# Optimization experiments

Hardware: AMD Instinct MI355X
Metric: run time of the kernel (lower is better)

## Reference

```python
import jax, jax.numpy as jnp
import numpy as np
import math

NUM_HEADS = 8
LN_EPS = 1e-5


def layer_norm(x, g, b):
    mu = x.mean(-1, keepdims=True)
    var = ((x - mu) ** 2).mean(-1, keepdims=True)
    return (x - mu) * jax.lax.rsqrt(var + LN_EPS) * g + b


def typed_linear(x, W, types):
    # x: [E, in], W: [R, in, out], types: [E] int -> [E, out]
    out = jnp.zeros((x.shape[0], W.shape[-1]), x.dtype)
    for r in range(W.shape[0]):  # small fixed relation count
        out = out + jnp.where((types == r)[:, None], x @ W[r], 0.0)
    return out


def setup_inputs() -> dict:
    key = jax.random.key(0)
    ks = jax.random.split(key, 20)
    N, M, E = 50000, 10000, 100000
    in_dim, e_dim, out_dim, td = 128, 32, 128, 32
    R, T = 8, 4
    inp = {
        'src_h': jax.random.normal(ks[0], (N, in_dim), jnp.float32),
        'src_tw': jax.random.normal(ks[1], (N, td), jnp.float32),
        'src_tb': jax.random.normal(ks[2], (N, td), jnp.float32),
        'edge_h': jax.random.normal(ks[3], (E, e_dim), jnp.float32),
        'date': jax.random.uniform(ks[4], (E,), jnp.float32),
        'src_idx': jax.random.randint(ks[5], (E,), 0, N, jnp.int32),
        'dst_idx': jax.random.randint(ks[6], (E,), 0, M, jnp.int32),
        'etype': jax.random.randint(ks[7], (E,), 0, R, jnp.int32),
        'ntype': jax.random.randint(ks[8], (M,), 0, T, jnp.int32),
    }
    def w(k, shape):
        return jax.random.normal(k, shape, jnp.float32) / math.sqrt(shape[-2])
    inp['Wq'] = w(ks[9], (R, in_dim, out_dim))
    inp['Wk'] = w(ks[10], (R, in_dim + e_dim, out_dim))
    inp['Wv'] = w(ks[11], (R, in_dim + e_dim, out_dim))
    inp['Wa'] = w(ks[12], (T, out_dim, out_dim))
    inp['h_bias'] = jnp.zeros((T, out_dim), jnp.float32)
    inp['skip'] = jnp.ones((T,), jnp.float32)
    inp['src_ln_g'] = jnp.ones((in_dim + e_dim,), jnp.float32)
    inp['src_ln_b'] = jnp.zeros((in_dim + e_dim,), jnp.float32)
    inp['dst_ln_g'] = jnp.ones((in_dim,), jnp.float32)
    inp['dst_ln_b'] = jnp.zeros((in_dim,), jnp.float32)
    return inp


def reference(src_h, src_tw, src_tb, edge_h, date, src_idx, dst_idx, etype, ntype,
              Wq, Wk, Wv, Wa, h_bias, skip, src_ln_g, src_ln_b, dst_ln_g, dst_ln_b):
    M = ntype.shape[0]
    out_dim = Wq.shape[-1]
    H = NUM_HEADS
    hs = out_dim // H
    td = src_tw.shape[-1]
    t = date[:, None]  # [E,1]

    # gather src / dst node data per edge (dst nodes are first M src rows)
    h_s, tw_s, tb_s = src_h[src_idx], src_tw[src_idx], src_tb[src_idx]
    h_d, tw_d, tb_d = src_h[dst_idx], src_tw[dst_idx], src_tb[dst_idx]

    # time2vec modulation of the first td channels
    dia_s = jnp.concatenate([jnp.sin(tw_s * t + tb_s) * h_s[:, :td], h_s[:, td:]], -1)
    dia_d = jnp.concatenate([jnp.sin(tw_d * t + tb_d) * h_d[:, :td], h_d[:, td:]], -1)
    dia_s = jnp.concatenate([dia_s, edge_h], -1)  # [E, in_dim+e_dim]

    # pre_norm
    dia_s = layer_norm(dia_s, src_ln_g, src_ln_b)
    dia_d = layer_norm(dia_d, dst_ln_g, dst_ln_b)

    q = typed_linear(dia_d, Wq, etype).reshape(-1, H, hs)
    k = typed_linear(dia_s, Wk, etype).reshape(-1, H, hs)
    v = typed_linear(dia_s, Wv, etype).reshape(-1, H, hs)

    a = (q * k).sum(-1) / math.sqrt(out_dim)  # [E, H]

    # edge_softmax: segment softmax over destination nodes
    amax = jax.lax.stop_gradient(jax.ops.segment_max(a, dst_idx, num_segments=M))
    ex = jnp.exp(a - amax[dst_idx])
    denom = jax.ops.segment_sum(ex, dst_idx, num_segments=M)
    alpha = ex / denom[dst_idx]  # [E, H]

    # weighted scatter-sum aggregation
    m = (v * alpha[..., None]).reshape(-1, out_dim)  # [E, out_dim]
    h = jax.ops.segment_sum(m, dst_idx, num_segments=M)  # [M, out_dim]

    h = h + h_bias[ntype]
    gate = jax.nn.sigmoid(skip[ntype])[:, None]
    h = typed_linear(h, Wa, ntype)  # dropout is identity at eval
    dst_h = src_h[:M]
    return h * gate + dst_h * (1.0 - gate)
```

## Files before the change

kernel.cpp:

```cpp
#include <hip/hip_runtime.h>


typedef __attribute__((ext_vector_type(8))) short short8;
typedef __attribute__((ext_vector_type(4))) float f32x4;

__device__ __forceinline__ unsigned short f2bf(float f){
  union { float f; unsigned u; } x; x.f = f;
  unsigned r = x.u + 0x7FFFu + ((x.u >> 16) & 1u);
  return (unsigned short)(r >> 16);
}
__device__ __forceinline__ float bf2f(unsigned short b){
  union { unsigned u; float f; } x; x.u = ((unsigned)b) << 16;
  return x.f;
}
__device__ __forceinline__ float wred(float v){
  #pragma unroll
  for(int i=1;i<64;i<<=1) v += __shfl_xor(v, i);
  return v;
}


__global__ void k_zero(int* __restrict__ p, int n){
  int i = blockIdx.x*256 + threadIdx.x;
  if(i < n) p[i] = 0;
}

__global__ __launch_bounds__(256) void k_hist(
    const int* __restrict__ etype, const int* __restrict__ dst_idx,
    const int* __restrict__ ntype,
    int* cnt_e, int* cnt_d, int* cnt_n, int E, int M){
  __shared__ int le[8], ln[4];
  int tid = threadIdx.x;
  if(tid < 8) le[tid] = 0;
  if(tid < 4) ln[tid] = 0;
  __syncthreads();
  int g = blockIdx.x*256 + tid;
  if(g < E){ atomicAdd(&le[etype[g]], 1); atomicAdd(&cnt_d[dst_idx[g]], 1); }
  if(g < M){ atomicAdd(&ln[ntype[g]], 1); }
  __syncthreads();
  if(tid < 8 && le[tid]) atomicAdd(&cnt_e[tid], le[tid]);
  if(tid < 4 && ln[tid]) atomicAdd(&cnt_n[tid], ln[tid]);
}

__global__ __launch_bounds__(1024) void k_scan(const int* __restrict__ cnt_e, int* off_e,
                                               const int* __restrict__ cnt_n, int* off_n,
                                               const int* __restrict__ cnt_d, int* off_d, int M){
  __shared__ int part[1024];
  int tid = threadIdx.x;
  if(tid == 0){
    int s = 0;
    for(int i=0;i<8;i++){ off_e[i]=s; s+=cnt_e[i]; } off_e[8]=s;
    s = 0;
    for(int i=0;i<4;i++){ off_n[i]=s; s+=cnt_n[i]; } off_n[4]=s;
  }
  int per = (M + 1023) >> 10;
  int s = 0;
  for(int j=0;j<per;j++){ int idx = tid*per + j; if(idx < M) s += cnt_d[idx]; }
  part[tid] = s; __syncthreads();
  for(int o=1;o<1024;o<<=1){
    int v = (tid >= o) ? part[tid-o] : 0;
    __syncthreads();
    part[tid] += v;
    __syncthreads();
  }
  int run = (tid == 0) ? 0 : part[tid-1];
  for(int j=0;j<per;j++){
    int idx = tid*per + j;
    if(idx < M){ off_d[idx] = run; run += cnt_d[idx]; }
  }
  if(tid == 1023) off_d[M] = run;
}

__global__ __launch_bounds__(256) void k_scatter(
    const int* __restrict__ etype, const int* __restrict__ dst_idx,
    const int* __restrict__ ntype,
    const int* __restrict__ off_e, int* cur_e,
    const int* __restrict__ off_d, int* cur_d,
    const int* __restrict__ off_n, int* cur_n,
    int* eperm, int* dstlist, int* nperm, int* npos, int E, int M){
  __shared__ int lcnt[8], lbase[8], lnc[4], lnb[4];
  int tid = threadIdx.x;
  if(tid < 8) lcnt[tid] = 0;
  if(tid < 4) lnc[tid] = 0;
  __syncthreads();
  int g = blockIdx.x*256 + tid;
  int r = 0, lrank = 0, t = 0, nrank = 0;
  bool inE = (g < E), inM = (g < M);
  if(inE){ r = etype[g]; lrank = atomicAdd(&lcnt[r], 1); }
  if(inM){ t = ntype[g]; nrank = atomicAdd(&lnc[t], 1); }
  __syncthreads();
  if(tid < 8 && lcnt[tid]) lbase[tid] = atomicAdd(&cur_e[tid], lcnt[tid]);
  if(tid < 4 && lnc[tid])  lnb[tid]   = atomicAdd(&cur_n[tid], lnc[tid]);
  __syncthreads();
  if(inE){
    int p = off_e[r] + lbase[r] + lrank;
    eperm[p] = g;
    int d = dst_idx[g];
    int q = off_d[d] + atomicAdd(&cur_d[d], 1);
    dstlist[q] = p;
  }
  if(inM){
    int np = off_n[t] + lnb[t] + nrank;
    npos[g] = np;
    nperm[np] = g;
  }
}

__global__ void k_convw(const float* __restrict__ Wq, const float* __restrict__ Wk,
                        const float* __restrict__ Wv, const float* __restrict__ Wa,
                        unsigned short* Wq_t, unsigned short* Wk_t,
                        unsigned short* Wv_t, unsigned short* Wa_t){
  int tid = blockIdx.x*256 + threadIdx.x;
  if(tid < 131072){
    int r = tid >> 14, rem = tid & 16383, k = rem >> 7, n = rem & 127;
    int nb=n>>4, m=n&15, c=k>>5, quad=(k>>3)&3, j=k&7;
    Wq_t[r*16384 + ((nb*4 + c)*4 + quad)*128 + m*8 + j] = f2bf(Wq[tid]);
  } else if(tid < 294912){
    int u = tid - 131072;
    int r = u / 20480, rem = u - r*20480, k = rem >> 7, n = rem & 127;
    int nb=n>>4, m=n&15, c=k>>5, quad=(k>>3)&3, j=k&7;
    Wk_t[r*20480 + ((nb*5 + c)*4 + quad)*128 + m*8 + j] = f2bf(Wk[u]);
  } else if(tid < 458752){
    int u = tid - 294912;
    int r = u / 20480, rem = u - r*20480, k = rem >> 7, n = rem & 127;
    int nb=n>>4, m=n&15, c=k>>5, quad=(k>>3)&3, j=k&7;
    Wv_t[r*20480 + ((nb*5 + c)*4 + quad)*128 + m*8 + j] = f2bf(Wv[u]);
  } else if(tid < 524288){
    int u = tid - 458752;
    int r = u >> 14, rem = u & 16383, k = rem >> 7, n = rem & 127;
    int nb=n>>4, m=n&15, c=k>>5, quad=(k>>3)&3, j=k&7;
    Wa_t[r*16384 + ((nb*4 + c)*4 + quad)*128 + m*8 + j] = f2bf(Wa[u]);
  }
}

__global__ __launch_bounds__(256) void k_prep(
  const float* __restrict__ src_h, const float* __restrict__ src_tw, const float* __restrict__ src_tb,
  const float* __restrict__ edge_h, const float* __restrict__ date,
  const int* __restrict__ src_idx, const int* __restrict__ dst_idx, const int* __restrict__ eperm,
  const float* __restrict__ g_s, const float* __restrict__ b_s,
  const float* __restrict__ g_d, const float* __restrict__ b_d,
  unsigned short* __restrict__ dia_s, unsigned short* __restrict__ dia_d, int E)
{
  int p = blockIdx.x*4 + (threadIdx.x >> 6);
  if(p >= E) return;
  int lane = threadIdx.x & 63;
  int e = eperm[p];
  float t = date[e];
  int s = src_idx[e], d = dst_idx[e];
  {
    float h0 = src_h[(size_t)s*128 + lane];
    float h1 = src_h[(size_t)s*128 + 64 + lane];
    float x0 = h0, x2 = 0.f;
    if(lane < 32){
      x0 = __sinf(src_tw[s*32 + lane]*t + src_tb[s*32 + lane]) * h0;
      x2 = edge_h[(size_t)e*32 + lane];
    }
    float x1 = h1;
    float mu = wred(x0 + x1 + x2) * (1.f/160.f);
    float d0 = x0-mu, d1 = x1-mu, d2 = (lane<32) ? (x2-mu) : 0.f;
    float var = wred(d0*d0 + d1*d1 + d2*d2) * (1.f/160.f);
    float sc = rsqrtf(var + 1e-5f);
    size_t bo = (size_t)p*160;
    dia_s[bo + lane]      = f2bf(d0*sc*g_s[lane]      + b_s[lane]);
    dia_s[bo + 64 + lane] = f2bf(d1*sc*g_s[64+lane]   + b_s[64+lane]);
    if(lane < 32)
      dia_s[bo + 128 + lane] = f2bf(d2*sc*g_s[128+lane] + b_s[128+lane]);
  }
  {
    float h0 = src_h[(size_t)d*128 + lane];
    float h1 = src_h[(size_t)d*128 + 64 + lane];
    float x0 = (lane < 32) ? __sinf(src_tw[d*32+lane]*t + src_tb[d*32+lane]) * h0 : h0;
    float x1 = h1;
    float mu = wred(x0 + x1) * (1.f/128.f);
    float d0 = x0-mu, d1 = x1-mu;
    float var = wred(d0*d0 + d1*d1) * (1.f/128.f);
    float sc = rsqrtf(var + 1e-5f);
    size_t bo = (size_t)p*128;
    dia_d[bo + lane]      = f2bf(d0*sc*g_d[lane]    + b_d[lane]);
    dia_d[bo + 64 + lane] = f2bf(d1*sc*g_d[64+lane] + b_d[64+lane]);
  }
}

template<int NC>
__device__ __forceinline__ void gemm64r(
  const unsigned short* __restrict__ A, int lda,
  const unsigned short* __restrict__ Wf,
  f32x4* acc, int tid)
{
  int lane = tid & 63, w = tid >> 6, m = lane & 15, quad = lane >> 4;
  const unsigned short* p0 = Wf + (size_t)(2*w)*NC*512 + lane*8;
  short8 b0[NC], b1[NC];
  #pragma unroll
  for(int c=0;c<NC;c++){
    b0[c] = *(const short8*)(p0 + c*512);
    b1[c] = *(const short8*)(p0 + NC*512 + c*512);
  }
  #pragma unroll
  for(int i=0;i<8;i++) acc[i] = (f32x4){0.f,0.f,0.f,0.f};
  #pragma unroll
  for(int c=0;c<NC;c++){
    #pragma unroll
    for(int rt=0; rt<4; rt++){
      short8 af = *(const short8*)(A + (rt*16 + m)*lda + c*32 + quad*8);
      acc[rt*2+0] = __builtin_amdgcn_mfma_f32_16x16x32_bf16(af, b0[c], acc[rt*2+0], 0,0,0);
      acc[rt*2+1] = __builtin_amdgcn_mfma_f32_16x16x32_bf16(af, b1[c], acc[rt*2+1], 0,0,0);
    }
  }
}

__global__ __launch_bounds__(256) void k_qkv(
  const unsigned short* __restrict__ dia_d, const unsigned short* __restrict__ dia_s,
  const unsigned short* __restrict__ Wq_t, const unsigned short* __restrict__ Wk_t,
  const unsigned short* __restrict__ Wv_t,
  const int* __restrict__ cnt_e, const int* __restrict__ off_e,
  float* __restrict__ abuf, unsigned short* __restrict__ vbuf)
{
  __shared__ unsigned short Ad[64*136];
  __shared__ unsigned short As[64*168];
  int bid = blockIdx.x;
  int r = -1, tl0 = 0, accT = 0;
  #pragma unroll
  for(int i=0;i<8;i++){
    int n = cnt_e[i], tt = (n + 63) >> 6;
    if(r < 0 && bid < accT + tt){ r = i; tl0 = bid - accT; }
    accT += tt;
  }
  if(r < 0) return;
  int row0 = off_e[r] + tl0*64;
  int nv = min(64, cnt_e[r] - tl0*64);
  int tid = threadIdx.x;
  {
    int4 z = make_int4(0,0,0,0);
    #pragma unroll
    for(int it=0; it<4; it++){
      int idx = it*256 + tid, row = idx >> 4, c = idx & 15;
      int4 v = z;
      if(row < nv) v = *(const int4*)(dia_d + (size_t)(row0+row)*128 + c*8);
      *(int4*)(Ad + row*136 + c*8) = v;
    }
    #pragma unroll
    for(int it=0; it<5; it++){
      int idx = it*256 + tid, row = idx/20, c = idx%20;
      int4 v = z;
      if(row < nv) v = *(const int4*)(dia_s + (size_t)(row0+row)*160 + c*8);
      *(int4*)(As + row*168 + c*8) = v;
    }
  }
  __syncthreads();
  int lane = tid & 63, w = tid >> 6, m = lane & 15, quad = lane >> 4;
  f32x4 q[8], kk[8], vv[8];
  gemm64r<4>(Ad, 136, Wq_t + r*16384, q,  tid);
  gemm64r<5>(As, 168, Wk_t + r*20480, kk, tid);
  const float inv = 0.08838834764831845f;
  #pragma unroll
  for(int rt=0; rt<4; rt++)
  #pragma unroll
  for(int ct=0; ct<2; ct++){
    #pragma unroll
    for(int reg=0; reg<4; reg++){
      float s = q[rt*2+ct][reg] * kk[rt*2+ct][reg];
      s += __shfl_xor(s,1); s += __shfl_xor(s,2); s += __shfl_xor(s,4); s += __shfl_xor(s,8);
      int row = rt*16 + quad*4 + reg;
      if(m == 0 && row < nv) abuf[(size_t)(row0+row)*8 + w*2 + ct] = s * inv;
    }
  }
  gemm64r<5>(As, 168, Wv_t + r*20480, vv, tid);
  #pragma unroll
  for(int rt=0; rt<4; rt++)
  #pragma unroll
  for(int ct=0; ct<2; ct++)
  #pragma unroll
  for(int reg=0; reg<4; reg++){
    int row = rt*16 + quad*4 + reg;
    if(row < nv)
      vbuf[(size_t)(row0+row)*128 + w*32 + ct*16 + m] = f2bf(vv[rt*2+ct][reg]);
  }
}

__global__ __launch_bounds__(128) void k_aggr(
  const float* __restrict__ abuf, const unsigned short* __restrict__ vbuf,
  const int* __restrict__ dstlist, const int* __restrict__ off_d,
  const int* __restrict__ npos, const int* __restrict__ ntype,
  const float* __restrict__ h_bias, unsigned short* __restrict__ hpre)
{
  int d = blockIdx.x, tid = threadIdx.x;
  int o0 = off_d[d], cnt = off_d[d+1] - o0;
  __shared__ float den[8];
  if(tid < 8) den[tid] = 0.f;
  __syncthreads();
  for(int idx = tid; idx < cnt*8; idx += 128){
    int i = idx >> 3, h = idx & 7;
    float ex = __expf(abuf[(size_t)dstlist[o0+i]*8 + h]);
    atomicAdd(&den[h], ex);
  }
  __syncthreads();
  int h = tid >> 4;
  float dh = den[h];
  float rd = (dh > 0.f) ? (1.f/dh) : 0.f;
  float acc = 0.f;
  for(int i=0; i<cnt; i++){
    int p = dstlist[o0+i];
    float al = __expf(abuf[(size_t)p*8 + h]) * rd;
    acc += al * bf2f(vbuf[(size_t)p*128 + tid]);
  }
  int t = ntype[d];
  acc += h_bias[t*128 + tid];
  hpre[(size_t)npos[d]*128 + tid] = f2bf(acc);
}

__global__ __launch_bounds__(256) void k_final(
  const unsigned short* __restrict__ hpre, const unsigned short* __restrict__ Wa_t,
  const int* __restrict__ cnt_n, const int* __restrict__ off_n, const int* __restrict__ nperm,
  const float* __restrict__ skip, const float* __restrict__ src_h, float* __restrict__ out)
{
  __shared__ unsigned short Ah[64*136];
  int bid = blockIdx.x;
  int r = -1, tl0 = 0, accT = 0;
  #pragma unroll
  for(int i=0;i<4;i++){
    int n = cnt_n[i], tt = (n + 63) >> 6;
    if(r < 0 && bid < accT + tt){ r = i; tl0 = bid - accT; }
    accT += tt;
  }
  if(r < 0) return;
  int row0 = off_n[r] + tl0*64;
  int nv = min(64, cnt_n[r] - tl0*64);
  float gate = 1.f / (1.f + __expf(-skip[r]));
  int tid = threadIdx.x;
  int4 z = make_int4(0,0,0,0);
  #pragma unroll
  for(int it=0; it<4; it++){
    int idx = it*256 + tid, row = idx >> 4, c = idx & 15;
    int4 v = z;
    if(row < nv) v = *(const int4*)(hpre + (size_t)(row0+row)*128 + c*8);
    *(int4*)(Ah + row*136 + c*8) = v;
  }
  __syncthreads();
  f32x4 acc[8];
  gemm64r<4>(Ah, 136, Wa_t + r*16384, acc, tid);
  int lane = tid & 63, w = tid >> 6, m = lane & 15, quad = lane >> 4;
  #pragma unroll
  for(int rt=0; rt<4; rt++)
  #pragma unroll
  for(int ct=0; ct<2; ct++)
  #pragma unroll
  for(int reg=0; reg<4; reg++){
    int row = rt*16 + quad*4 + reg;
    if(row < nv){
      int dd = nperm[row0+row];
      int col = w*32 + ct*16 + m;
      out[(size_t)dd*128 + col] = acc[rt*2+ct][reg]*gate + src_h[(size_t)dd*128 + col]*(1.f - gate);
    }
  }
}

extern "C" void kernel_launch(void* const* d_in, const int* in_sizes, int n_in,
                              void* d_out, int out_size, void* d_ws, size_t ws_size,
                              hipStream_t stream)
{
  const float* src_h  = (const float*)d_in[0];
  const float* src_tw = (const float*)d_in[1];
  const float* src_tb = (const float*)d_in[2];
  const float* edge_h = (const float*)d_in[3];
  const float* date   = (const float*)d_in[4];
  const int*   src_idx= (const int*)d_in[5];
  const int*   dst_idx= (const int*)d_in[6];
  const int*   etype  = (const int*)d_in[7];
  const int*   ntype  = (const int*)d_in[8];
  const float* Wq     = (const float*)d_in[9];
  const float* Wk     = (const float*)d_in[10];
  const float* Wv     = (const float*)d_in[11];
  const float* Wa     = (const float*)d_in[12];
  const float* h_bias = (const float*)d_in[13];
  const float* skip   = (const float*)d_in[14];
  const float* g_s    = (const float*)d_in[15];
  const float* b_s    = (const float*)d_in[16];
  const float* g_d    = (const float*)d_in[17];
  const float* b_d    = (const float*)d_in[18];
  float* out = (float*)d_out;

  const int E = in_sizes[4];
  const int M = in_sizes[8];

  char* base = (char*)d_ws;
  size_t off = 0;
  auto alloc = [&](size_t bytes)->char*{
    off = (off + 255) & ~(size_t)255;
    char* p = base + off; off += bytes; return p;
  };
  int* cnt_e = (int*)alloc((size_t)(24 + 2*M)*4);
  int* cur_e = cnt_e + 8;
  int* cnt_n = cur_e + 8;
  int* cur_n = cnt_n + 4;
  int* cnt_d = cur_n + 4;
  int* cur_d = cnt_d + M;
  const int nzero = 24 + 2*M;
  int* off_e = (int*)alloc(9*4);
  int* off_n = (int*)alloc(5*4);
  int* off_d = (int*)alloc((size_t)(M+1)*4);
  int* eperm   = (int*)alloc((size_t)E*4);
  int* dstlist = (int*)alloc((size_t)E*4);
  int* nperm   = (int*)alloc((size_t)M*4);
  int* npos    = (int*)alloc((size_t)M*4);
  unsigned short* Wq_t = (unsigned short*)alloc((size_t)8*128*128*2);
  unsigned short* Wk_t = (unsigned short*)alloc((size_t)8*160*128*2);
  unsigned short* Wv_t = (unsigned short*)alloc((size_t)8*160*128*2);
  unsigned short* Wa_t = (unsigned short*)alloc((size_t)4*128*128*2);
  unsigned short* dia_d = (unsigned short*)alloc((size_t)E*128*2);
  unsigned short* dia_s = (unsigned short*)alloc((size_t)E*160*2);
  unsigned short* vbuf  = (unsigned short*)alloc((size_t)E*128*2);
  unsigned short* hpre  = (unsigned short*)alloc((size_t)M*128*2);
  float* abuf = (float*)alloc((size_t)E*8*4);

  k_zero<<<dim3((nzero+255)/256), dim3(256), 0, stream>>>(cnt_e, nzero);
  k_hist<<<dim3((E+255)/256), dim3(256), 0, stream>>>(etype, dst_idx, ntype, cnt_e, cnt_d, cnt_n, E, M);
  k_scan<<<dim3(1), dim3(1024), 0, stream>>>(cnt_e, off_e, cnt_n, off_n, cnt_d, off_d, M);
  k_scatter<<<dim3((E+255)/256), dim3(256), 0, stream>>>(etype, dst_idx, ntype,
      off_e, cur_e, off_d, cur_d, off_n, cur_n, eperm, dstlist, nperm, npos, E, M);
  k_convw<<<dim3(2048), dim3(256), 0, stream>>>(Wq, Wk, Wv, Wa, Wq_t, Wk_t, Wv_t, Wa_t);
  k_prep<<<dim3((E+3)/4), dim3(256), 0, stream>>>(src_h, src_tw, src_tb, edge_h, date,
      src_idx, dst_idx, eperm, g_s, b_s, g_d, b_d, dia_s, dia_d, E);
  k_qkv<<<dim3(E/64 + 9), dim3(256), 0, stream>>>(dia_d, dia_s, Wq_t, Wk_t, Wv_t,
      cnt_e, off_e, abuf, vbuf);
  k_aggr<<<dim3(M), dim3(128), 0, stream>>>(abuf, vbuf, dstlist, off_d, npos, ntype, h_bias, hpre);
  k_final<<<dim3(M/64 + 5), dim3(256), 0, stream>>>(hpre, Wa_t, cnt_n, off_n, nperm, skip, src_h, out);
}
```

Before: 284.8 us.

## Fuse time-encoding and layer-norm prep into the QKV GEMM kernel

Drops the separate k_prep kernel and its bf16 dia_s/dia_d intermediate buffers. The QKV kernel now gathers the source and destination features itself, applies the sin time encoding and both layer norms, and writes the bf16 rows straight into shared memory. Layer norm switches to single-pass sum and sum-of-squares reductions interleaved across four values. This removes one launch and the global write and reread of the intermediates. In exchange, the gather latency now sits inside the GEMM blocks and may hurt latency hiding, and the E[x^2]-mu^2 variance form is less numerically robust.

```diff
diff --git a/kernel.cpp b/kernel.cpp
--- a/kernel.cpp
+++ b/kernel.cpp
@@ -12,11 +12,6 @@
 __device__ __forceinline__ float bf2f(unsigned short b){
   union { unsigned u; float f; } x; x.u = ((unsigned)b) << 16;
   return x.f;
-}
-__device__ __forceinline__ float wred(float v){
-  #pragma unroll
-  for(int i=1;i<64;i<<=1) v += __shfl_xor(v, i);
-  return v;
 }
 
 
@@ -133,54 +128,6 @@
   }
 }
 
-__global__ __launch_bounds__(256) void k_prep(
-  const float* __restrict__ src_h, const float* __restrict__ src_tw, const float* __restrict__ src_tb,
-  const float* __restrict__ edge_h, const float* __restrict__ date,
-  const int* __restrict__ src_idx, const int* __restrict__ dst_idx, const int* __restrict__ eperm,
-  const float* __restrict__ g_s, const float* __restrict__ b_s,
-  const float* __restrict__ g_d, const float* __restrict__ b_d,
-  unsigned short* __restrict__ dia_s, unsigned short* __restrict__ dia_d, int E)
-{
-  int p = blockIdx.x*4 + (threadIdx.x >> 6);
-  if(p >= E) return;
-  int lane = threadIdx.x & 63;
-  int e = eperm[p];
-  float t = date[e];
-  int s = src_idx[e], d = dst_idx[e];
-  {
-    float h0 = src_h[(size_t)s*128 + lane];
-    float h1 = src_h[(size_t)s*128 + 64 + lane];
-    float x0 = h0, x2 = 0.f;
-    if(lane < 32){
-      x0 = __sinf(src_tw[s*32 + lane]*t + src_tb[s*32 + lane]) * h0;
-      x2 = edge_h[(size_t)e*32 + lane];
-    }
-    float x1 = h1;
-    float mu = wred(x0 + x1 + x2) * (1.f/160.f);
-    float d0 = x0-mu, d1 = x1-mu, d2 = (lane<32) ? (x2-mu) : 0.f;
-    float var = wred(d0*d0 + d1*d1 + d2*d2) * (1.f/160.f);
-    float sc = rsqrtf(var + 1e-5f);
-    size_t bo = (size_t)p*160;
-    dia_s[bo + lane]      = f2bf(d0*sc*g_s[lane]      + b_s[lane]);
-    dia_s[bo + 64 + lane] = f2bf(d1*sc*g_s[64+lane]   + b_s[64+lane]);
-    if(lane < 32)
-      dia_s[bo + 128 + lane] = f2bf(d2*sc*g_s[128+lane] + b_s[128+lane]);
-  }
-  {
-    float h0 = src_h[(size_t)d*128 + lane];
-    float h1 = src_h[(size_t)d*128 + 64 + lane];
-    float x0 = (lane < 32) ? __sinf(src_tw[d*32+lane]*t + src_tb[d*32+lane]) * h0 : h0;
-    float x1 = h1;
-    float mu = wred(x0 + x1) * (1.f/128.f);
-    float d0 = x0-mu, d1 = x1-mu;
-    float var = wred(d0*d0 + d1*d1) * (1.f/128.f);
-    float sc = rsqrtf(var + 1e-5f);
-    size_t bo = (size_t)p*128;
-    dia_d[bo + lane]      = f2bf(d0*sc*g_d[lane]    + b_d[lane]);
-    dia_d[bo + 64 + lane] = f2bf(d1*sc*g_d[64+lane] + b_d[64+lane]);
-  }
-}
-
 template<int NC>
 __device__ __forceinline__ void gemm64r(
   const unsigned short* __restrict__ A, int lda,
@@ -209,7 +156,11 @@
 }
 
 __global__ __launch_bounds__(256) void k_qkv(
-  const unsigned short* __restrict__ dia_d, const unsigned short* __restrict__ dia_s,
+  const float* __restrict__ src_h, const float* __restrict__ src_tw, const float* __restrict__ src_tb,
+  const float* __restrict__ edge_h, const float* __restrict__ date,
+  const int* __restrict__ src_idx, const int* __restrict__ dst_idx, const int* __restrict__ eperm,
+  const float* __restrict__ g_s, const float* __restrict__ b_s,
+  const float* __restrict__ g_d, const float* __restrict__ b_d,
   const unsigned short* __restrict__ Wq_t, const unsigned short* __restrict__ Wk_t,
   const unsigned short* __restrict__ Wv_t,
   const int* __restrict__ cnt_e, const int* __restrict__ off_e,
@@ -229,25 +180,66 @@
   int row0 = off_e[r] + tl0*64;
   int nv = min(64, cnt_e[r] - tl0*64);
   int tid = threadIdx.x;
+  int lane = tid & 63, w = tid >> 6, m = lane & 15, quad = lane >> 4;
+
   {
-    int4 z = make_int4(0,0,0,0);
-    #pragma unroll
-    for(int it=0; it<4; it++){
-      int idx = it*256 + tid, row = idx >> 4, c = idx & 15;
-      int4 v = z;
-      if(row < nv) v = *(const int4*)(dia_d + (size_t)(row0+row)*128 + c*8);
-      *(int4*)(Ad + row*136 + c*8) = v;
+    float2 gs01 = *(const float2*)(g_s + 2*lane);
+    float2 bs01 = *(const float2*)(b_s + 2*lane);
+    float2 gd01 = *(const float2*)(g_d + 2*lane);
+    float2 bd01 = *(const float2*)(b_d + 2*lane);
+    float gs2 = 0.f, bs2 = 0.f;
+    if(lane < 32){ gs2 = g_s[128+lane]; bs2 = b_s[128+lane]; }
+    for(int row = w; row < 64; row += 4){
+      unsigned* as_pair = (unsigned*)(As + row*168);
+      unsigned* ad_pair = (unsigned*)(Ad + row*136);
+      if(row < nv){
+        int e = eperm[row0 + row];
+        float t = date[e];
+        int s = src_idx[e], d = dst_idx[e];
+        float2 hs = *(const float2*)(src_h + (size_t)s*128 + 2*lane);
+        float2 hd = *(const float2*)(src_h + (size_t)d*128 + 2*lane);
+        float xe = 0.f;
+        if(lane < 32) xe = edge_h[(size_t)e*32 + lane];
+        float sx0 = hs.x, sx1 = hs.y, dx0 = hd.x, dx1 = hd.y;
+        if(lane < 16){
+          float2 tws = *(const float2*)(src_tw + (size_t)s*32 + 2*lane);
+          float2 tbs = *(const float2*)(src_tb + (size_t)s*32 + 2*lane);
+          float2 twd = *(const float2*)(src_tw + (size_t)d*32 + 2*lane);
+          float2 tbd = *(const float2*)(src_tb + (size_t)d*32 + 2*lane);
+          sx0 = __sinf(tws.x*t + tbs.x) * hs.x;
+          sx1 = __sinf(tws.y*t + tbs.y) * hs.y;
+          dx0 = __sinf(twd.x*t + tbd.x) * hd.x;
+          dx1 = __sinf(twd.y*t + tbd.y) * hd.y;
+        }
+        float s1 = sx0 + sx1 + xe;
+        float s2 = sx0*sx0 + sx1*sx1 + xe*xe;
+        float t1 = dx0 + dx1;
+        float t2 = dx0*dx0 + dx1*dx1;
+        #pragma unroll
+        for(int i=1;i<64;i<<=1){
+          s1 += __shfl_xor(s1,i); s2 += __shfl_xor(s2,i);
+          t1 += __shfl_xor(t1,i); t2 += __shfl_xor(t2,i);
+        }
+        float smu = s1*(1.f/160.f);
+        float ssc = rsqrtf(s2*(1.f/160.f) - smu*smu + 1e-5f);
+        float dmu = t1*(1.f/128.f);
+        float dsc = rsqrtf(t2*(1.f/128.f) - dmu*dmu + 1e-5f);
+        unsigned short y0 = f2bf((sx0-smu)*ssc*gs01.x + bs01.x);
+        unsigned short y1 = f2bf((sx1-smu)*ssc*gs01.y + bs01.y);
+        as_pair[lane] = (unsigned)y0 | ((unsigned)y1 << 16);
+        if(lane < 32) As[row*168 + 128 + lane] = f2bf((xe-smu)*ssc*gs2 + bs2);
+        unsigned short z0 = f2bf((dx0-dmu)*dsc*gd01.x + bd01.x);
+        unsigned short z1 = f2bf((dx1-dmu)*dsc*gd01.y + bd01.y);
+        ad_pair[lane] = (unsigned)z0 | ((unsigned)z1 << 16);
+      } else {
+        as_pair[lane] = 0u;
+        if(lane < 32) As[row*168 + 128 + lane] = 0;
+        ad_pair[lane] = 0u;
+      }
     }
-    #pragma unroll
-    for(int it=0; it<5; it++){
-      int idx = it*256 + tid, row = idx/20, c = idx%20;
-      int4 v = z;
-      if(row < nv) v = *(const int4*)(dia_s + (size_t)(row0+row)*160 + c*8);
-      *(int4*)(As + row*168 + c*8) = v;
-    }
-  }
-  __syncthreads();
-  int lane = tid & 63, w = tid >> 6, m = lane & 15, quad = lane >> 4;
+  }
+  __syncthreads();
+
   f32x4 q[8], kk[8], vv[8];
   gemm64r<4>(Ad, 136, Wq_t + r*16384, q,  tid);
   gemm64r<5>(As, 168, Wk_t + r*20480, kk, tid);
@@ -406,8 +398,6 @@
   unsigned short* Wk_t = (unsigned short*)alloc((size_t)8*160*128*2);
   unsigned short* Wv_t = (unsigned short*)alloc((size_t)8*160*128*2);
   unsigned short* Wa_t = (unsigned short*)alloc((size_t)4*128*128*2);
-  unsigned short* dia_d = (unsigned short*)alloc((size_t)E*128*2);
-  unsigned short* dia_s = (unsigned short*)alloc((size_t)E*160*2);
   unsigned short* vbuf  = (unsigned short*)alloc((size_t)E*128*2);
   unsigned short* hpre  = (unsigned short*)alloc((size_t)M*128*2);
   float* abuf = (float*)alloc((size_t)E*8*4);
@@ -418,10 +408,9 @@
   k_scatter<<<dim3((E+255)/256), dim3(256), 0, stream>>>(etype, dst_idx, ntype,
       off_e, cur_e, off_d, cur_d, off_n, cur_n, eperm, dstlist, nperm, npos, E, M);
   k_convw<<<dim3(2048), dim3(256), 0, stream>>>(Wq, Wk, Wv, Wa, Wq_t, Wk_t, Wv_t, Wa_t);
-  k_prep<<<dim3((E+3)/4), dim3(256), 0, stream>>>(src_h, src_tw, src_tb, edge_h, date,
-      src_idx, dst_idx, eperm, g_s, b_s, g_d, b_d, dia_s, dia_d, E);
-  k_qkv<<<dim3(E/64 + 9), dim3(256), 0, stream>>>(dia_d, dia_s, Wq_t, Wk_t, Wv_t,
-      cnt_e, off_e, abuf, vbuf);
+  k_qkv<<<dim3(E/64 + 9), dim3(256), 0, stream>>>(src_h, src_tw, src_tb, edge_h, date,
+      src_idx, dst_idx, eperm, g_s, b_s, g_d, b_d,
+      Wq_t, Wk_t, Wv_t, cnt_e, off_e, abuf, vbuf);
   k_aggr<<<dim3(M), dim3(128), 0, stream>>>(abuf, vbuf, dstlist, off_d, npos, ntype, h_bias, hpre);
   k_final<<<dim3(M/64 + 5), dim3(256), 0, stream>>>(hpre, Wa_t, cnt_n, off_n, nperm, skip, src_h, out);
 }
```

New measurement: 311.1 us. 9.2% more time.
